# Kernel optimization log

Measured on AMD Instinct MI355X. Metric: run time of the kernel, lower is better.

The kernel has to match this reference:

```python
import jax, jax.numpy as jnp
import numpy as np

B, N = 256, 512          # trees, nodes per tree (topological order, root last)
IN, HID, OUT = 57, 512, 57  # len(ascii_letters + " .,;'") = 57


def setup_inputs() -> dict:
    rng = np.random.default_rng(0)
    # children indices strictly less than node index; -1 means absent child
    u = rng.random((B, N, 2))
    idx = np.arange(N)[None, :, None]
    ch = np.floor(u * (idx + 1)).astype(np.int32) - 1  # in [-1, i-1]
    left_idx = jnp.asarray(ch[..., 0])
    right_idx = jnp.asarray(ch[..., 1])
    values = jnp.asarray(rng.integers(0, IN, (B, N)), dtype=jnp.int32)
    key = jax.random.key(0)
    k1, k2, k3, k4 = jax.random.split(key, 4)
    s1 = 1.0 / np.sqrt(IN + HID)
    s2 = 1.0 / np.sqrt(HID)
    W_ih = jax.random.uniform(k1, (IN + HID, HID), minval=-s1, maxval=s1, dtype=jnp.float32)
    b_ih = jax.random.uniform(k2, (HID,), minval=-s1, maxval=s1, dtype=jnp.float32)
    W_o = jax.random.uniform(k3, (HID, OUT), minval=-s2, maxval=s2, dtype=jnp.float32)
    b_o = jax.random.uniform(k4, (OUT,), minval=-s2, maxval=s2, dtype=jnp.float32)
    return dict(left_idx=left_idx, right_idx=right_idx, values=values,
                W_ih=W_ih, b_ih=b_ih, W_o=W_o, b_o=b_o)


def _encode(left_idx, right_idx, values, W_ih, b_ih):
    # one-hot chars, precompute the input half of the concat+linear for all nodes
    X = jax.nn.one_hot(values, IN, dtype=W_ih.dtype)        # [B,N,IN]
    Wx, Wh = W_ih[:IN], W_ih[IN:]                            # split concat linear
    Xp = jnp.einsum('bni,ih->bnh', X, Wx) + b_ih             # [B,N,HID]
    SENT = N  # sentinel row holding zeros (hidden for None child)
    li = jnp.where(left_idx < 0, SENT, left_idx)             # [B,N]
    ri = jnp.where(right_idx < 0, SENT, right_idx)
    H0 = jnp.zeros((B, N + 1, HID), Xp.dtype)
    brange = jnp.arange(B)

    def step(H, inp):
        i, xp, l, r = inp                                    # xp:[B,HID], l/r:[B]
        hl = H[brange, l]                                    # gather child hiddens
        hr = H[brange, r]
        h = jnp.tanh(xp + (hl + hr) @ Wh)                    # recurrence
        H = H.at[:, i].set(h)
        return H, None

    xs = (jnp.arange(N), jnp.swapaxes(Xp, 0, 1), li.T, ri.T)
    H, _ = jax.lax.scan(step, H0, xs)
    return H[:, N - 1]                                       # root hidden [B,HID]


def reference(left_idx, right_idx, values, W_ih, b_ih, W_o, b_o):
    h_root = _encode(left_idx, right_idx, values, W_ih, b_ih)
    logits = h_root @ W_o + b_o                              # i2o
    return jax.nn.log_softmax(logits, axis=1)                # [B,OUT]
```

## Files before the change

kernel.cpp:

```cpp
#include <hip/hip_runtime.h>
#include <stdint.h>

#define BATCH 256
#define NNODE 512
#define INP   57
#define HIDD  512
#define OUTD  57
#define SENTOFF (NNODE * HIDD)

typedef int i32x4 __attribute__((ext_vector_type(4)));

__global__ void pack_wq(const float* __restrict__ W_ih, const float* __restrict__ b_ih,
                        signed char* __restrict__ Wq){
  int idx = blockIdx.x * 256 + threadIdx.x;
  int j    =  idx        & 15;
  int lane = (idx >> 4)  & 63;
  int nt   = (idx >> 10) & 31;
  int kt   =  idx >> 15;
  int n    = nt * 16 + (lane & 15);
  int ksub = (lane >> 4) * 16 + j;
  const float scale = 127.0f * sqrtf((float)(INP + HIDD));
  float wv; float sc = scale;
  if (kt < 8) {
    const int ktrue = kt * 64 + 16 * (ksub & 3) + (ksub >> 2);
    wv = W_ih[(size_t)(INP + ktrue) * HIDD + n];
  } else {
    sc = scale * 0.5f;
    if (ksub < INP)       wv = W_ih[(size_t)ksub * HIDD + n];
    else if (ksub == INP) wv = b_ih[n];
    else                  wv = 0.0f;
  }
  float q = rintf(wv * sc);
  q = fminf(127.0f, fmaxf(-127.0f, q));
  Wq[idx] = (signed char)q;
}

__device__ __forceinline__ unsigned int avg_s8x4(unsigned int a, unsigned int b){
  unsigned int au = a ^ 0x80808080u, bu = b ^ 0x80808080u;
  unsigned int o = au | bu, x = au ^ bu;
  return ((o - ((x >> 1) & 0x7F7F7F7Fu)) ^ 0x80808080u);
}

struct Pref { uint4 l[2]; uint4 r[2]; };

__device__ __forceinline__ void load_pref_safe(
    Pref& p, int m0, int Mcur, int w, int m16, int quad,
    const int* ord_s, const int* li_s, const int* ri_s, const int* hot_s,
    const signed char* Hb)
{
  const int koff = w * 64 + quad * 16;
  #pragma unroll
  for (int mt = 0; mt < 2; ++mt) {
    const int row  = mt * 16 + m16;
    const bool live = row < Mcur;
    const int pos  = m0 + row;
    const int node = live ? ord_s[pos] : -1;
    const int hb   = live ? hot_s[pos] : 0;
    const int loff = (node >= 0) ? li_s[node] : SENTOFF;
    const int roff = (node >= 0) ? ri_s[node] : SENTOFF;
    if (!(hb & 1)) p.l[mt] = *(const uint4*)(Hb + (size_t)(loff + koff));
    if (!(hb & 2)) p.r[mt] = *(const uint4*)(Hb + (size_t)(roff + koff));
  }
}

__device__ __forceinline__ void write_pref(
    const Pref& p, int m0, int Mcur, int w, int lane, int m16, int quad,
    signed char* __restrict__ Ab, const int* ord_s, const int* val_s)
{
  #pragma unroll
  for (int mt = 0; mt < 2; ++mt) {
    uint4 o;
    o.x = avg_s8x4(p.l[mt].x, p.r[mt].x);
    o.y = avg_s8x4(p.l[mt].y, p.r[mt].y);
    o.z = avg_s8x4(p.l[mt].z, p.r[mt].z);
    o.w = avg_s8x4(p.l[mt].w, p.r[mt].w);
    *(uint4*)(Ab + (w * 2 + mt) * 1024 + lane * 16) = o;
  }
  if (w < 2) {
    const int erow  = w * 16 + m16;
    const int enode = (erow < Mcur) ? ord_s[m0 + erow] : -1;
    const int v     = (enode >= 0) ? val_s[enode] : -1;
    signed char bytes[16];
    #pragma unroll
    for (int j = 0; j < 16; ++j) {
      const int ks = quad * 16 + j;
      bytes[j] = (enode >= 0 && (ks == v || ks == INP)) ? (signed char)127 : (signed char)0;
    }
    *(i32x4*)(Ab + (16 + w) * 1024 + lane * 16) = *(const i32x4*)bytes;
  }
}

__device__ __forceinline__ void patch_and_write(
    Pref& p, int m0, int Mcur, int w, int lane, int m16, int quad,
    signed char* __restrict__ Ab,
    const int* ord_s, const int* li_s, const int* ri_s, const int* val_s,
    const int* hot_s, const signed char* Hb)
{
  const int koff = w * 64 + quad * 16;
  #pragma unroll
  for (int mt = 0; mt < 2; ++mt) {
    const int row  = mt * 16 + m16;
    const bool live = row < Mcur;
    const int pos  = m0 + row;
    const int hb   = live ? hot_s[pos] : 0;
    if (hb) {
      const int node = ord_s[pos];
      if (hb & 1) p.l[mt] = *(const uint4*)(Hb + (size_t)(li_s[node] + koff));
      if (hb & 2) p.r[mt] = *(const uint4*)(Hb + (size_t)(ri_s[node] + koff));
    }
  }
  write_pref(p, m0, Mcur, w, lane, m16, quad, Ab, ord_s, val_s);
}

#define SCLE_VAL (5.7707801635558536f / (16129.0f * 23.853720883753127f))

__device__ __forceinline__ int tanh_q(int accv){
  const float x  = (float)accv * SCLE_VAL;
  const float e  = __builtin_amdgcn_exp2f(x);
  const float r  = __builtin_amdgcn_rcpf(e + 1.0f);
  return __float2int_rn(fmaf(-254.0f, r, 127.0f));
}

template<int NMT>
__device__ __forceinline__ void compute_chunk(
    int m0, int Mcur, int w, int lane, int m16, int quad,
    const signed char* __restrict__ Ab,
    const int* ordoff_s, const i32x4 (&Bv)[9][4], signed char* Hb)
{
  i32x4 acc[NMT][4];
  #pragma unroll
  for (int mt = 0; mt < NMT; ++mt)
    #pragma unroll
    for (int nt = 0; nt < 4; ++nt)
      acc[mt][nt] = (i32x4){0, 0, 0, 0};

  #pragma unroll
  for (int kt = 0; kt < 8; ++kt) {
    #pragma unroll
    for (int mt = 0; mt < NMT; ++mt) {
      i32x4 a = *(const i32x4*)(Ab + (kt * 2 + mt) * 1024 + lane * 16);
      #pragma unroll
      for (int nt = 0; nt < 4; ++nt)
        acc[mt][nt] = __builtin_amdgcn_mfma_i32_16x16x64_i8(a, Bv[kt][nt], acc[mt][nt], 0, 0, 0);
    }
  }
  #pragma unroll
  for (int mt = 0; mt < NMT; ++mt) {
    i32x4 ax = *(const i32x4*)(Ab + (16 + mt) * 1024 + lane * 16);
    #pragma unroll
    for (int nt = 0; nt < 4; ++nt)
      acc[mt][nt] = __builtin_amdgcn_mfma_i32_16x16x64_i8(ax, Bv[8][nt], acc[mt][nt], 0, 0, 0);
  }

  #pragma unroll
  for (int mt = 0; mt < NMT; ++mt) {
    #pragma unroll
    for (int rg = 0; rg < 4; ++rg) {
      const int rowc = mt * 16 + quad * 4 + rg;
      if (rowc < Mcur) {
        const int q0 = tanh_q(acc[mt][0][rg]) & 255;
        const int q1 = tanh_q(acc[mt][1][rg]) & 255;
        const int q2 = tanh_q(acc[mt][2][rg]) & 255;
        const int q3 = tanh_q(acc[mt][3][rg]);
        const int packed = q0 | (q1 << 8) | (q2 << 16) | (q3 << 24);
        *(int*)(Hb + (size_t)ordoff_s[m0 + rowc] + (w * 64 + m16 * 4)) = packed;
      }
    }
  }
}

__global__ __launch_bounds__(512, 2) void tree_rnn(
    const int* __restrict__ left, const int* __restrict__ right,
    const int* __restrict__ values,
    const float* __restrict__ W_ih, const float* __restrict__ b_ih,
    const float* __restrict__ W_o,  const float* __restrict__ b_o,
    const signed char* __restrict__ Wq,
    signed char* __restrict__ Hbuf, float* __restrict__ out)
{
  __shared__ __align__(16) signed char Abuf[2][18 * 1024];
  __shared__ int li_s[NNODE], ri_s[NNODE], val_s[NNODE];
  __shared__ int lvl_s[NNODE], ord_s[NNODE], ordoff_s[NNODE], hot_s[NNODE];
  __shared__ int cnt_s[NNODE], cnt2_s[NNODE];
  __shared__ int offs_s[NNODE + 1];
  __shared__ int cdesc_s[NNODE];
  __shared__ int chg_s, lmax_s, nc_s;
  __shared__ float hroot_s[HIDD];
  __shared__ float red_s[OUTD][8];
  __shared__ float logit_s[64];

  const int b    = blockIdx.x;
  const int tid  = threadIdx.x;
  const int lane = tid & 63;
  const int w    = tid >> 6;
  signed char* Hb = Hbuf + (size_t)b * (NNODE + 1) * HIDD;

  li_s[tid]  = left  [b * NNODE + tid];
  ri_s[tid]  = right [b * NNODE + tid];
  val_s[tid] = values[b * NNODE + tid];
  lvl_s[tid] = 0; cnt_s[tid] = 0; cnt2_s[tid] = 0;
  if (tid < 128) ((unsigned int*)(Hb + (size_t)NNODE * HIDD))[tid] = 0;
  if (tid == 0) lmax_s = 0;
  __syncthreads();

  for (;;) {
    if (tid == 0) chg_s = 0;
    __syncthreads();
    {
      int l = li_s[tid], r = ri_s[tid];
      int dl = (l >= 0) ? lvl_s[l] : -1;
      int dr = (r >= 0) ? lvl_s[r] : -1;
      int nl = 1 + (dl > dr ? dl : dr);
      if (nl > lvl_s[tid]) { lvl_s[tid] = nl; chg_s = 1; }
    }
    __syncthreads();
    if (!chg_s) break;
  }

  const int myl = lvl_s[tid];
  {
    int ml = myl;
    #pragma unroll
    for (int m = 1; m < 64; m <<= 1) ml = max(ml, __shfl_xor(ml, m, 64));
    if (lane == 0) atomicMax(&lmax_s, ml);
    atomicAdd(&cnt_s[myl], 1);
  }
  __syncthreads();
  const int Lmax = lmax_s;
  if (tid == 0) {
    int acc = 0;
    for (int L = 0; L <= Lmax; ++L) { offs_s[L] = acc; acc += cnt_s[L]; }
    offs_s[Lmax + 1] = acc;
    int nc = 0;
    for (int L = 0; L <= Lmax; ++L)
      for (int m0 = offs_s[L]; m0 < offs_s[L + 1]; m0 += 32) {
        int sz = min(32, offs_s[L + 1] - m0);
        cdesc_s[nc++] = m0 | (sz << 16) | ((m0 == offs_s[L]) ? (1 << 30) : 0);
      }
    nc_s = nc;
  }
  __syncthreads();
  {
    int pos = offs_s[myl] + atomicAdd(&cnt2_s[myl], 1);
    ord_s[pos] = tid;
    ordoff_s[pos] = tid * HIDD;
  }
  __syncthreads();
  {
    const int node = ord_s[tid];
    const int L = lvl_s[node];
    const int l = li_s[node], r = ri_s[node];
    const bool first = (tid - offs_s[L]) < 32;
    int h = 0;
    if (first && l >= 0 && lvl_s[l] == L - 1) h |= 1;
    if (first && r >= 0 && lvl_s[r] == L - 1) h |= 2;
    hot_s[tid] = h;
  }
  __syncthreads();
  {
    int l = li_s[tid], r = ri_s[tid];
    li_s[tid] = (l < 0 ? NNODE : l) * HIDD;
    ri_s[tid] = (r < 0 ? NNODE : r) * HIDD;
  }
  __syncthreads();

  const int m16  = lane & 15;
  const int quad = lane >> 4;

  i32x4 Bv[9][4];
  #pragma unroll
  for (int kt = 0; kt < 9; ++kt)
    #pragma unroll
    for (int nt = 0; nt < 4; ++nt)
      Bv[kt][nt] = *(const i32x4*)(Wq + ((size_t)(kt * 32 + 4 * w + nt) * 64 + lane) * 16);

  const int NC = nc_s;
  Pref p;
  {
    const int d = cdesc_s[0];
    load_pref_safe(p, d & 0xFFFF, (d >> 16) & 0x3FFF, w, m16, quad,
                   ord_s, li_s, ri_s, hot_s, Hb);
  }
  for (int gc = 0; gc < NC; ++gc) {
    const int d  = cdesc_s[gc];
    const int m0 = d & 0xFFFF, Mc = (d >> 16) & 0x3FFF;
    const bool first = (d >> 30) & 1;
    __syncthreads();
    if (first) {
      patch_and_write(p, m0, Mc, w, lane, m16, quad, Abuf[gc & 1],
                      ord_s, li_s, ri_s, val_s, hot_s, Hb);
      __syncthreads();
    }
    const bool more = gc + 1 < NC;
    Pref pn; int m01 = 0, Mc1 = 0; bool f1 = false;
    if (more) {
      const int d1 = cdesc_s[gc + 1];
      m01 = d1 & 0xFFFF; Mc1 = (d1 >> 16) & 0x3FFF; f1 = (d1 >> 30) & 1;
      load_pref_safe(pn, m01, Mc1, w, m16, quad, ord_s, li_s, ri_s, hot_s, Hb);
    }
    const signed char* Ab = Abuf[gc & 1];
    if (Mc > 16)
      compute_chunk<2>(m0, Mc, w, lane, m16, quad, Ab, ordoff_s, Bv, Hb);
    else
      compute_chunk<1>(m0, Mc, w, lane, m16, quad, Ab, ordoff_s, Bv, Hb);
    if (more && !f1)
      write_pref(pn, m01, Mc1, w, lane, m16, quad, Abuf[(gc + 1) & 1], ord_s, val_s);
    p = pn;
  }
  __syncthreads();

  {
    const int t6 = tid & 63;
    const int tt = (tid & ~63) | (((t6 & 3) << 4) | (t6 >> 2));
    hroot_s[tt] = (float)Hb[(size_t)(NNODE - 1) * HIDD + tid] * (1.0f / 127.0f);
  }
  __syncthreads();
  {
    const int j = tid >> 3, part = tid & 7;
    if (j < OUTD) {
      float p2 = 0.f;
      const int k0 = part * 64;
      for (int k = k0; k < k0 + 64; ++k)
        p2 += hroot_s[k] * W_o[(size_t)k * OUTD + j];
      red_s[j][part] = p2;
    }
  }
  __syncthreads();
  if (tid < OUTD) {
    float s = b_o[tid];
    #pragma unroll
    for (int pp = 0; pp < 8; ++pp) s += red_s[tid][pp];
    logit_s[tid] = s;
  }
  __syncthreads();
  if (w == 0) {
    float x = (lane < OUTD) ? logit_s[lane] : -1e30f;
    float mx = x;
    #pragma unroll
    for (int m = 1; m < 64; m <<= 1) mx = fmaxf(mx, __shfl_xor(mx, m, 64));
    float ex = (lane < OUTD) ? __expf(x - mx) : 0.f;
    float sm = ex;
    #pragma unroll
    for (int m = 1; m < 64; m <<= 1) sm += __shfl_xor(sm, m, 64);
    float ls = logf(sm);
    if (lane < OUTD) out[b * OUTD + lane] = x - mx - ls;
  }
}

extern "C" void kernel_launch(void* const* d_in, const int* in_sizes, int n_in,
                              void* d_out, int out_size, void* d_ws, size_t ws_size,
                              hipStream_t stream) {
  const int*   left   = (const int*)  d_in[0];
  const int*   right  = (const int*)  d_in[1];
  const int*   values = (const int*)  d_in[2];
  const float* W_ih   = (const float*)d_in[3];
  const float* b_ih   = (const float*)d_in[4];
  const float* W_o    = (const float*)d_in[5];
  const float* b_o    = (const float*)d_in[6];
  float* out = (float*)d_out;

  signed char* Wq   = (signed char*)d_ws;
  signed char* Hbuf = (signed char*)((char*)d_ws + 512 * 1024);

  pack_wq<<<1152, 256, 0, stream>>>(W_ih, b_ih, Wq);
  tree_rnn<<<BATCH, 512, 0, stream>>>(left, right, values, W_ih, b_ih, W_o, b_o,
                                      Wq, Hbuf, out);
}
```

Before: 204.9 us.

## Mirror small-level hidden states in LDS and relax non-level-boundary barriers

When a tree level holds at most 32 nodes, its freshly computed hidden rows are also written to a shared-memory mirror. The next level's patch step then reads child hiddens from that mirror instead of re-reading global memory that was just written. This removes a global read-after-write round trip on the level-to-level critical path. Barriers between chunks within a level are replaced by an LDS-only wait plus s_barrier, which avoids waiting on outstanding global memory ops. The risks are extra LDS usage, which may lower occupancy, and correctness depending on the relaxed barrier still ordering the global writes that are read later.

Measured after the change: 214.6 us. +4.7%, slower.

```diff
diff --git a/kernel.cpp b/kernel.cpp
--- a/kernel.cpp
+++ b/kernel.cpp
@@ -35,6 +35,12 @@
   Wq[idx] = (signed char)q;
 }
 
+__device__ __forceinline__ void relaxed_barrier(){
+  asm volatile("s_waitcnt lgkmcnt(0)" ::: "memory");
+  __builtin_amdgcn_s_barrier();
+  __builtin_amdgcn_sched_barrier(0);
+}
+
 __device__ __forceinline__ unsigned int avg_s8x4(unsigned int a, unsigned int b){
   unsigned int au = a ^ 0x80808080u, bu = b ^ 0x80808080u;
   unsigned int o = au | bu, x = au ^ bu;
@@ -94,7 +100,7 @@
     Pref& p, int m0, int Mcur, int w, int lane, int m16, int quad,
     signed char* __restrict__ Ab,
     const int* ord_s, const int* li_s, const int* ri_s, const int* val_s,
-    const int* hot_s, const signed char* Hb)
+    const int* hot_s, const signed char* Hb, const signed char* Hmir)
 {
   const int koff = w * 64 + quad * 16;
   #pragma unroll
@@ -103,10 +109,16 @@
     const bool live = row < Mcur;
     const int pos  = m0 + row;
     const int hb   = live ? hot_s[pos] : 0;
-    if (hb) {
+    if (hb & 3) {
       const int node = ord_s[pos];
-      if (hb & 1) p.l[mt] = *(const uint4*)(Hb + (size_t)(li_s[node] + koff));
-      if (hb & 2) p.r[mt] = *(const uint4*)(Hb + (size_t)(ri_s[node] + koff));
+      if (hb & 1)
+        p.l[mt] = (hb & 4)
+          ? *(const uint4*)(Hmir + ((hb >> 8) & 63) * 512 + koff)
+          : *(const uint4*)(Hb + (size_t)(li_s[node] + koff));
+      if (hb & 2)
+        p.r[mt] = (hb & 8)
+          ? *(const uint4*)(Hmir + ((hb >> 16) & 63) * 512 + koff)
+          : *(const uint4*)(Hb + (size_t)(ri_s[node] + koff));
     }
   }
   write_pref(p, m0, Mcur, w, lane, m16, quad, Ab, ord_s, val_s);
@@ -125,7 +137,8 @@
 __device__ __forceinline__ void compute_chunk(
     int m0, int Mcur, int w, int lane, int m16, int quad,
     const signed char* __restrict__ Ab,
-    const int* ordoff_s, const i32x4 (&Bv)[9][4], signed char* Hb)
+    const int* ordoff_s, const i32x4 (&Bv)[9][4], signed char* Hb,
+    bool mir, signed char* __restrict__ Hmir)
 {
   i32x4 acc[NMT][4];
   #pragma unroll
@@ -163,7 +176,9 @@
         const int q2 = tanh_q(acc[mt][2][rg]) & 255;
         const int q3 = tanh_q(acc[mt][3][rg]);
         const int packed = q0 | (q1 << 8) | (q2 << 16) | (q3 << 24);
-        *(int*)(Hb + (size_t)ordoff_s[m0 + rowc] + (w * 64 + m16 * 4)) = packed;
+        const int col = w * 64 + m16 * 4;
+        *(int*)(Hb + (size_t)ordoff_s[m0 + rowc] + col) = packed;
+        if (mir) *(int*)(Hmir + rowc * 512 + col) = packed;
       }
     }
   }
@@ -178,8 +193,10 @@
     signed char* __restrict__ Hbuf, float* __restrict__ out)
 {
   __shared__ __align__(16) signed char Abuf[2][18 * 1024];
+  __shared__ __align__(16) signed char Hmir_s[32 * 512];
   __shared__ int li_s[NNODE], ri_s[NNODE], val_s[NNODE];
-  __shared__ int lvl_s[NNODE], ord_s[NNODE], ordoff_s[NNODE], hot_s[NNODE];
+  __shared__ int lvl_s[NNODE], ord_s[NNODE], ordoff_s[NNODE];
+  __shared__ int hot_s[NNODE], pos_s[NNODE];
   __shared__ int cnt_s[NNODE], cnt2_s[NNODE];
   __shared__ int offs_s[NNODE + 1];
   __shared__ int cdesc_s[NNODE];
@@ -234,7 +251,12 @@
     for (int L = 0; L <= Lmax; ++L)
       for (int m0 = offs_s[L]; m0 < offs_s[L + 1]; m0 += 32) {
         int sz = min(32, offs_s[L + 1] - m0);
-        cdesc_s[nc++] = m0 | (sz << 16) | ((m0 == offs_s[L]) ? (1 << 30) : 0);
+        int fl = 0;
+        if (m0 == offs_s[L]) {
+          fl |= (1 << 30);
+          if (offs_s[L + 1] - offs_s[L] <= 32) fl |= (1 << 29);
+        }
+        cdesc_s[nc++] = m0 | (sz << 16) | fl;
       }
     nc_s = nc;
   }
@@ -243,6 +265,7 @@
     int pos = offs_s[myl] + atomicAdd(&cnt2_s[myl], 1);
     ord_s[pos] = tid;
     ordoff_s[pos] = tid * HIDD;
+    pos_s[tid] = pos;
   }
   __syncthreads();
   {
@@ -250,9 +273,16 @@
     const int L = lvl_s[node];
     const int l = li_s[node], r = ri_s[node];
     const bool first = (tid - offs_s[L]) < 32;
+    const bool pmir = (L >= 1) && (offs_s[L] - offs_s[L - 1] <= 32);
     int h = 0;
-    if (first && l >= 0 && lvl_s[l] == L - 1) h |= 1;
-    if (first && r >= 0 && lvl_s[r] == L - 1) h |= 2;
+    if (first && l >= 0 && lvl_s[l] == L - 1) {
+      h |= 1;
+      if (pmir) h |= 4 | ((pos_s[l] - offs_s[L - 1]) << 8);
+    }
+    if (first && r >= 0 && lvl_s[r] == L - 1) {
+      h |= 2;
+      if (pmir) h |= 8 | ((pos_s[r] - offs_s[L - 1]) << 16);
+    }
     hot_s[tid] = h;
   }
   __syncthreads();
@@ -277,31 +307,33 @@
   Pref p;
   {
     const int d = cdesc_s[0];
-    load_pref_safe(p, d & 0xFFFF, (d >> 16) & 0x3FFF, w, m16, quad,
+    load_pref_safe(p, d & 0xFFFF, (d >> 16) & 0xFF, w, m16, quad,
                    ord_s, li_s, ri_s, hot_s, Hb);
   }
   for (int gc = 0; gc < NC; ++gc) {
     const int d  = cdesc_s[gc];
-    const int m0 = d & 0xFFFF, Mc = (d >> 16) & 0x3FFF;
+    const int m0 = d & 0xFFFF, Mc = (d >> 16) & 0xFF;
     const bool first = (d >> 30) & 1;
-    __syncthreads();
+    const bool mir   = (d >> 29) & 1;
+    if (first) __syncthreads();
+    else       relaxed_barrier();
     if (first) {
       patch_and_write(p, m0, Mc, w, lane, m16, quad, Abuf[gc & 1],
-                      ord_s, li_s, ri_s, val_s, hot_s, Hb);
-      __syncthreads();
+                      ord_s, li_s, ri_s, val_s, hot_s, Hb, Hmir_s);
+      relaxed_barrier();
     }
     const bool more = gc + 1 < NC;
     Pref pn; int m01 = 0, Mc1 = 0; bool f1 = false;
     if (more) {
       const int d1 = cdesc_s[gc + 1];
-      m01 = d1 & 0xFFFF; Mc1 = (d1 >> 16) & 0x3FFF; f1 = (d1 >> 30) & 1;
+      m01 = d1 & 0xFFFF; Mc1 = (d1 >> 16) & 0xFF; f1 = (d1 >> 30) & 1;
       load_pref_safe(pn, m01, Mc1, w, m16, quad, ord_s, li_s, ri_s, hot_s, Hb);
     }
     const signed char* Ab = Abuf[gc & 1];
     if (Mc > 16)
-      compute_chunk<2>(m0, Mc, w, lane, m16, quad, Ab, ordoff_s, Bv, Hb);
+      compute_chunk<2>(m0, Mc, w, lane, m16, quad, Ab, ordoff_s, Bv, Hb, mir, Hmir_s);
     else
-      compute_chunk<1>(m0, Mc, w, lane, m16, quad, Ab, ordoff_s, Bv, Hb);
+      compute_chunk<1>(m0, Mc, w, lane, m16, quad, Ab, ordoff_s, Bv, Hb, mir, Hmir_s);
     if (more && !f1)
       write_pref(pn, m01, Mc1, w, lane, m16, quad, Abuf[(gc + 1) & 1], ord_s, val_s);
     p = pn;
```
